# Optimization experiments

Hardware: AMD Instinct MI355X
Metric: run time of the kernel (lower is better)

Reference implementation:

```python
import jax, jax.numpy as jnp
import numpy as np

HIDDEN = 1024
NH = 16
NKV = 8
HD = 128
ROPE_BASE = 1e6
EPS = 1e-6


def _rms_norm(x, w):
    # x: [..., HD], norm in fp32 like the torch module
    xf = x.astype(jnp.float32)
    var = jnp.mean(xf * xf, axis=-1, keepdims=True)
    return w * (xf * jax.lax.rsqrt(var + EPS)).astype(x.dtype)


def _rotate_half(x):
    h = x.shape[-1] // 2
    return jnp.concatenate([-x[..., h:], x[..., :h]], axis=-1)


def _rope_cos_sin(position_ids, dtype):
    inv_freq = 1.0 / (ROPE_BASE ** (jnp.arange(0, HD, 2, dtype=jnp.float32) / HD))
    freqs = position_ids.astype(jnp.float32)[:, None] * inv_freq[None, :]  # [S, HD/2]
    emb = jnp.concatenate([freqs, freqs], axis=-1)  # [S, HD]
    return jnp.cos(emb).astype(dtype), jnp.sin(emb).astype(dtype)


def setup_inputs() -> dict:
    key = jax.random.key(0)
    ks = jax.random.split(key, 7)
    B, S = 2, 2048
    scale = lambda fan_in: 1.0 / np.sqrt(fan_in)
    return {
        "hidden_states": jax.random.normal(ks[0], (B, S, HIDDEN), jnp.float32),
        "position_ids": jnp.arange(S, dtype=jnp.int32),
        "Wq": jax.random.normal(ks[1], (HIDDEN, NH * HD), jnp.float32) * scale(HIDDEN),
        "Wk": jax.random.normal(ks[2], (HIDDEN, NKV * HD), jnp.float32) * scale(HIDDEN),
        "Wv": jax.random.normal(ks[3], (HIDDEN, NKV * HD), jnp.float32) * scale(HIDDEN),
        "Wo": jax.random.normal(ks[4], (NH * HD, HIDDEN), jnp.float32) * scale(NH * HD),
        "q_norm_w": jnp.ones((HD,), jnp.float32),
        "k_norm_w": jnp.ones((HD,), jnp.float32),
    }


def reference(hidden_states, position_ids, Wq, Wk, Wv, Wo, q_norm_w, k_norm_w):
    B, S, _ = hidden_states.shape
    G = NH // NKV  # GQA group size

    q = (hidden_states @ Wq).reshape(B, S, NH, HD)
    k = (hidden_states @ Wk).reshape(B, S, NKV, HD)
    v = (hidden_states @ Wv).reshape(B, S, NKV, HD)

    q = _rms_norm(q, q_norm_w).transpose(0, 2, 1, 3)  # [B, NH, S, HD]
    k = _rms_norm(k, k_norm_w).transpose(0, 2, 1, 3)  # [B, NKV, S, HD]
    v = v.transpose(0, 2, 1, 3)                        # [B, NKV, S, HD]

    cos, sin = _rope_cos_sin(position_ids, q.dtype)    # [S, HD] each
    q = q * cos + _rotate_half(q) * sin
    k = k * cos + _rotate_half(k) * sin

    # GQA: broadcast KV heads across groups instead of repeat_interleave copies
    qg = q.reshape(B, NKV, G, S, HD)
    scores = jnp.einsum('bkgsd,bknd->bkgsn', qg, k) / jnp.sqrt(jnp.float32(HD))
    causal = jnp.tril(jnp.ones((S, S), dtype=bool))
    scores = jnp.where(causal, scores, -jnp.inf)
    attn = jax.nn.softmax(scores, axis=-1)
    out = jnp.einsum('bkgsn,bknd->bkgsd', attn, v)  # [B, NKV, G, S, HD]
    out = out.reshape(B, NH, S, HD).transpose(0, 2, 1, 3).reshape(B, S, NH * HD)
    return out @ Wo
```

## Files before the change

### kernel.cpp

```cpp
#include <hip/hip_runtime.h>
#include <cstdint>
#include <cstddef>

#define HIDDEN 1024
#define NH 16
#define NKV 8
#define HD 128
#define SEQ 2048
#define BATCH 2
#define NTOK (BATCH*SEQ)

typedef __bf16 bf16x8 __attribute__((ext_vector_type(8)));
typedef float f32x4 __attribute__((ext_vector_type(4)));

__device__ __forceinline__ unsigned short f2bf(float f) {
  unsigned int u = __float_as_uint(f);
  u += 0x7FFFu + ((u >> 16) & 1u);
  return (unsigned short)(u >> 16);
}
__device__ __forceinline__ float bf2f(unsigned short h) {
  return __uint_as_float(((unsigned int)h) << 16);
}

#if __has_builtin(__builtin_amdgcn_exp2f)
#define EXP2(x) __builtin_amdgcn_exp2f(x)
#else
#define EXP2(x) exp2f(x)
#endif

__device__ __forceinline__ void glds16(const unsigned short* g, unsigned short* l) {
  __builtin_amdgcn_global_load_lds(
      (const __attribute__((address_space(1))) unsigned int*)g,
      (__attribute__((address_space(3))) unsigned int*)l, 16, 0, 0);
}

#define WAIT_VM8()   __builtin_amdgcn_s_waitcnt(0x0F78)
#define WAIT_VM4()   __builtin_amdgcn_s_waitcnt(0x0F74)
#define WAIT_VM0()   __builtin_amdgcn_s_waitcnt(0x0F70)
#define WAIT_LGKM0() __builtin_amdgcn_s_waitcnt(0xC07F)
#define BARRIER()    __builtin_amdgcn_s_barrier()

__device__ __forceinline__ float dpp_addx1(float x) {
  int v = __builtin_amdgcn_update_dpp(0, __float_as_int(x), 0xB1, 0xF, 0xF, true);
  return x + __int_as_float(v);
}

__global__ __launch_bounds__(256) void tcvt_all_kernel(
    const float* __restrict__ Wq, const float* __restrict__ Wk,
    const float* __restrict__ Wv, const float* __restrict__ Wo,
    const float* __restrict__ hs,
    unsigned short* __restrict__ wqkvt, unsigned short* __restrict__ wot,
    unsigned short* __restrict__ hsb) {
  const int i = blockIdx.x;
  const int tx = threadIdx.x, ty = threadIdx.y;
  if (i >= 6144) {
    const int t = ty*32 + tx;
    const size_t base = (size_t)(i - 6144) * 1024;
#pragma unroll
    for (int j = 0; j < 4; ++j) {
      const size_t idx = base + j*256 + t;
      float4 v = ((const float4*)hs)[idx];
      ushort4 o;
      o.x = f2bf(v.x); o.y = f2bf(v.y); o.z = f2bf(v.z); o.w = f2bf(v.w);
      ((ushort4*)hsb)[idx] = o;
    }
    return;
  }
  __shared__ float tl[32][33];
  const float* src; unsigned short* dst; int R, C, r0, c0;
  if (i < 2048)      { int l = i;        src = Wq; dst = wqkvt;                      R = 1024; C = 2048; r0 = (l & 31)*32; c0 = (l >> 5)*32; }
  else if (i < 3072) { int l = i - 2048; src = Wk; dst = wqkvt + (size_t)2048*1024;  R = 1024; C = 1024; r0 = (l & 31)*32; c0 = (l >> 5)*32; }
  else if (i < 4096) { int l = i - 3072; src = Wv; dst = wqkvt + (size_t)3072*1024;  R = 1024; C = 1024; r0 = (l & 31)*32; c0 = (l >> 5)*32; }
  else               { int l = i - 4096; src = Wo; dst = wot;                        R = 2048; C = 1024; r0 = (l & 63)*32; c0 = (l >> 6)*32; }
#pragma unroll
  for (int k = 0; k < 4; ++k)
    tl[ty + 8*k][tx] = src[(size_t)(r0 + ty + 8*k)*C + c0 + tx];
  __syncthreads();
#pragma unroll
  for (int k = 0; k < 4; ++k)
    dst[(size_t)(c0 + ty + 8*k)*R + r0 + tx] = f2bf(tl[tx][ty + 8*k]);
}

__global__ __launch_bounds__(256) void gemm_qkv_fused_kernel(
    const unsigned short* __restrict__ A,
    const unsigned short* __restrict__ Bt,
    const float* __restrict__ qw, const float* __restrict__ kw,
    const int* __restrict__ pos_ids,
    unsigned short* __restrict__ q_l,
    unsigned short* __restrict__ k_l,
    unsigned short* __restrict__ vt8) {
  constexpr int BM = 128, BK = 64, K = 1024, NIT = K/BK;
  constexpr int FS = 132;
  __shared__ __align__(16) char smem[70144];
  unsigned short* As0 = (unsigned short*)smem;
  unsigned short* Bs0 = (unsigned short*)(smem + 32768);
  float* ftile = (float*)smem;
  float* rinv  = (float*)(smem + 69632);

  const int t = threadIdx.x, lane = t & 63, w = t >> 6;
  const int l15 = lane & 15, l4 = lane >> 4;
  const int wr = (w >> 1)*64, wc = (w & 1)*64;
  const int m0 = blockIdx.x * BM, n0 = blockIdx.y * 128;
  const unsigned short* Ab = A + (size_t)m0*K;
  const unsigned short* Bb = Bt + (size_t)n0*K;

  const f32x4 vzero = {0.f, 0.f, 0.f, 0.f};
  f32x4 acc[4][4];
#pragma unroll
  for (int i = 0; i < 4; ++i)
#pragma unroll
    for (int j = 0; j < 4; ++j) acc[i][j] = vzero;

#pragma unroll
  for (int i = 0; i < 4; ++i) {
    const int c = (w*4 + i)*64 + lane;
    glds16(Ab + (size_t)(c >> 3)*K + (c & 7)*8, As0 + (size_t)(w*4 + i)*512);
  }
#pragma unroll
  for (int i = 0; i < 4; ++i) {
    const int c = (w*4 + i)*64 + lane;
    glds16(Bb + (size_t)(c >> 3)*K + (c & 7)*8, Bs0 + (size_t)(w*4 + i)*512);
  }

  for (int kb = 0; kb < NIT; ++kb) {
    const int cur = kb & 1;
    WAIT_LGKM0(); BARRIER();
    if (kb + 1 < NIT) {
      const int kn = (kb + 1) * BK;
      const int nb = (cur^1)*8192;
#pragma unroll
      for (int i = 0; i < 4; ++i) {
        const int c = (w*4 + i)*64 + lane;
        glds16(Ab + (size_t)(c >> 3)*K + kn + (c & 7)*8, As0 + nb + (size_t)(w*4 + i)*512);
      }
#pragma unroll
      for (int i = 0; i < 4; ++i) {
        const int c = (w*4 + i)*64 + lane;
        glds16(Bb + (size_t)(c >> 3)*K + kn + (c & 7)*8, Bs0 + nb + (size_t)(w*4 + i)*512);
      }
      WAIT_VM8();
    } else {
      WAIT_VM0();
    }
    BARRIER();

    const unsigned short* Ac = As0 + cur*8192;
    const unsigned short* Bc = Bs0 + cur*8192;
#pragma unroll
    for (int kk = 0; kk < 2; ++kk) {
      const int kc = kk*4 + l4;
      bf16x8 af[4], bfr[4];
#pragma unroll
      for (int i = 0; i < 4; ++i) {
        int m = wr + i*16 + l15;
        af[i] = *(const bf16x8*)(Ac + ((size_t)m*8 + kc)*8);
      }
#pragma unroll
      for (int j = 0; j < 4; ++j) {
        int n = wc + j*16 + l15;
        bfr[j] = *(const bf16x8*)(Bc + ((size_t)n*8 + kc)*8);
      }
#pragma unroll
      for (int i = 0; i < 4; ++i)
#pragma unroll
        for (int j = 0; j < 4; ++j)
          acc[i][j] = __builtin_amdgcn_mfma_f32_16x16x32_bf16(af[i], bfr[j], acc[i][j], 0, 0, 0);
    }
  }

  WAIT_LGKM0(); BARRIER();
#pragma unroll
  for (int i = 0; i < 4; ++i)
#pragma unroll
    for (int j = 0; j < 4; ++j)
#pragma unroll
      for (int r = 0; r < 4; ++r) {
        const int row = wr + i*16 + l4*4 + r;
        const int col = wc + j*16 + l15;
        ftile[row*FS + col] = acc[i][j][r];
      }
  WAIT_LGKM0(); BARRIER();

  const int ny = n0 >> 7;
  const int S0 = m0 & (SEQ-1);
  const int bb = m0 >> 11;

  if (ny < 24) {
    const bool isQ = ny < 16;
    {
      const int row = t >> 1, h2 = t & 1;
      const float* fr = ftile + row*FS + h2*64;
      float ssq = 0.f;
#pragma unroll
      for (int c = 0; c < 16; ++c) {
        float4 v = *(const float4*)(fr + 4*c);
        ssq += v.x*v.x + v.y*v.y + v.z*v.z + v.w*v.w;
      }
      ssq = dpp_addx1(ssq);
      if (h2 == 0) rinv[row] = rsqrtf(ssq*(1.0f/128.0f) + 1e-6f);
    }
    WAIT_LGKM0(); BARRIER();
    const float* wgt = isQ ? qw : kw;
    const int d = t & 127, rh = t >> 7;
    const float wd = wgt[d];
    const float w2 = wgt[d ^ 64];
    const float sgn = (d < 64) ? -1.f : 1.f;
    const float sOut = isQ ? 0.12751744f : 1.f;
    const float invf = exp2f(-(float)(d & 63) * 0.31143075889569023f);
    const int pos0 = pos_ids[S0 + rh*64];
    float cs, sn, dc, dsn;
    __sincosf((float)pos0 * invf, &sn, &cs);
    __sincosf(invf, &dsn, &dc);
    const int head = isQ ? ny : (ny - 16);
    unsigned short* dstb = isQ ? (q_l + ((size_t)(bb*NH + head)*SEQ + S0)*HD)
                               : (k_l + ((size_t)(bb*NKV + head)*SEQ + S0)*HD);
#pragma unroll 4
    for (int k = 0; k < 64; ++k) {
      const int row = rh*64 + k;
      const float r  = rinv[row];
      const float x1 = ftile[row*FS + d];
      const float x2 = ftile[row*FS + (d ^ 64)];
      const float y1 = x1*r*wd, y2 = x2*r*w2;
      const float o  = (y1*cs + sgn*(y2*sn)) * sOut;
      dstb[(size_t)row*HD + d] = f2bf(o);
      const float c2 = cs*dc - sn*dsn;
      sn = sn*dc + cs*dsn; cs = c2;
    }
  } else {
    const int vh = ny - 24;
    unsigned short* vb = vt8 + (size_t)(bb*NKV + vh)*HD*SEQ;
    const int d = t & 127, sbh = t >> 7;
#pragma unroll
    for (int sb = 0; sb < 8; ++sb) {
      const int sl = sbh*8 + sb;
      const int blk = sl >> 3, s = sl & 7;
      const int base_r = blk*64 + ((s>>2)<<5) + (((s>>1)&1)<<3) + ((s&1)<<2);
      union { unsigned short u[8]; uint4 q; } pk;
#pragma unroll
      for (int s8 = 0; s8 < 8; ++s8) {
        const int row = base_r + ((s8>>2)<<4) + (((s8>>1)&1)<<1) + (s8&1);
        pk.u[s8] = f2bf(ftile[row*FS + d]);
      }
      *(uint4*)(vb + ((size_t)((S0 >> 3) + sl)*128 + d)*8) = pk.q;
    }
  }
}

__global__ __launch_bounds__(256) void gemm_out_kernel(
    const unsigned short* __restrict__ A,
    const unsigned short* __restrict__ Bt,
    float* __restrict__ Cout, int M, int N, int K) {
  constexpr int BK = 64;
  __shared__ unsigned short As[2][128*BK];
  __shared__ unsigned short Bs[2][128*BK];
  const int t = threadIdx.x, lane = t & 63, w = t >> 6;
  const int l15 = lane & 15, l4 = lane >> 4;
  const int wr = (w >> 1)*64, wc = (w & 1)*64;
  const int m0 = blockIdx.y * 128, n0 = blockIdx.x * 128;
  const unsigned short* Ab = A + (size_t)m0*K;
  const unsigned short* Bb = Bt + (size_t)n0*K;

  const f32x4 vzero = {0.f, 0.f, 0.f, 0.f};
  f32x4 acc[4][4];
#pragma unroll
  for (int i = 0; i < 4; ++i)
#pragma unroll
    for (int j = 0; j < 4; ++j) acc[i][j] = vzero;

  const int NIT = K / BK;
#pragma unroll
  for (int i = 0; i < 4; ++i) {
    const int c = (w*4 + i)*64 + lane;
    glds16(Ab + (size_t)(c >> 3)*K + (c & 7)*8, &As[0][(size_t)(w*4 + i)*512]);
  }
#pragma unroll
  for (int i = 0; i < 4; ++i) {
    const int c = (w*4 + i)*64 + lane;
    glds16(Bb + (size_t)(c >> 3)*K + (c & 7)*8, &Bs[0][(size_t)(w*4 + i)*512]);
  }

  for (int kb = 0; kb < NIT; ++kb) {
    const int cur = kb & 1;
    WAIT_LGKM0(); BARRIER();
    if (kb + 1 < NIT) {
      const int kn = (kb + 1) * BK;
#pragma unroll
      for (int i = 0; i < 4; ++i) {
        const int c = (w*4 + i)*64 + lane;
        glds16(Ab + (size_t)(c >> 3)*K + kn + (c & 7)*8, &As[cur^1][(size_t)(w*4 + i)*512]);
      }
#pragma unroll
      for (int i = 0; i < 4; ++i) {
        const int c = (w*4 + i)*64 + lane;
        glds16(Bb + (size_t)(c >> 3)*K + kn + (c & 7)*8, &Bs[cur^1][(size_t)(w*4 + i)*512]);
      }
      WAIT_VM8();
    } else {
      WAIT_VM0();
    }
    BARRIER();

#pragma unroll
    for (int kk = 0; kk < 2; ++kk) {
      const int kc = kk*4 + l4;
      bf16x8 af[4], bfr[4];
#pragma unroll
      for (int i = 0; i < 4; ++i) {
        int m = wr + i*16 + l15;
        af[i] = *(const bf16x8*)(&As[cur][((size_t)m*8 + kc)*8]);
      }
#pragma unroll
      for (int j = 0; j < 4; ++j) {
        int n = wc + j*16 + l15;
        bfr[j] = *(const bf16x8*)(&Bs[cur][((size_t)n*8 + kc)*8]);
      }
#pragma unroll
      for (int i = 0; i < 4; ++i)
#pragma unroll
        for (int j = 0; j < 4; ++j)
          acc[i][j] = __builtin_amdgcn_mfma_f32_16x16x32_bf16(af[i], bfr[j], acc[i][j], 0, 0, 0);
    }
  }
#pragma unroll
  for (int i = 0; i < 4; ++i)
#pragma unroll
    for (int j = 0; j < 4; ++j)
#pragma unroll
      for (int r = 0; r < 4; ++r) {
        int row = m0 + wr + i*16 + l4*4 + r;
        int col = n0 + wc + j*16 + l15;
        Cout[(size_t)row*N + col] = acc[i][j][r];
      }
}

__global__ __launch_bounds__(256, 2) void attn_kernel(
    const unsigned short* __restrict__ q_l,
    const unsigned short* __restrict__ k_l,
    const unsigned short* __restrict__ vt8,
    unsigned short* __restrict__ o_part,
    float* __restrict__ l_part) {
  __shared__ __align__(16) char smem[65536];
  unsigned short* Ks0  = (unsigned short*)smem;
  unsigned short* Vts0 = (unsigned short*)(smem + 32768);

  const int t = threadIdx.x;
  const int lane = t & 63;
  const int w = t >> 6;
  const int l15 = lane & 15, l4 = lane >> 4;
  const int hb = blockIdx.x;
  const int h = hb & 15, b = hb >> 4;
  const int y = blockIdx.y;
  const int qt = 15 - (y >> 1);
  const int half = y & 1;
  const int kvh = h >> 1;
  const int q0 = qt * 128;
  const int kt0 = half ? (qt + 1) : 0;
  const int kt1 = half ? (2*qt + 2) : (qt + 1);

  const unsigned short* Kg = k_l + ((size_t)(b*NKV + kvh)*SEQ)*HD;
  const unsigned short* Vg = vt8 + (size_t)(b*NKV + kvh)*HD*SEQ;
  const unsigned short* Qbase = q_l + ((size_t)(b*NH + h)*SEQ)*HD;

  const f32x4 vzero = {0.f,0.f,0.f,0.f};

  bf16x8 qf[2][4];
#pragma unroll
  for (int i = 0; i < 2; ++i) {
    const int row = q0 + w*32 + i*16 + l15;
    const unsigned short* Qp = Qbase + (size_t)row*HD;
#pragma unroll
    for (int kk = 0; kk < 4; ++kk)
      qf[i][kk] = *(const bf16x8*)(Qp + kk*32 + l4*8);
  }

  f32x4 oacc[2][8];
#pragma unroll
  for (int i = 0; i < 2; ++i)
#pragma unroll
    for (int jd = 0; jd < 8; ++jd) oacc[i][jd] = vzero;
  float lrun[2] = {0.f, 0.f};

  {
    const int k00 = kt0 * 64;
#pragma unroll
    for (int i = 0; i < 4; ++i) {
      const int kc = w*4 + i;
      const int m = lane ^ (kc & 7);
      glds16(Kg + (size_t)(k00 + m)*HD + kc*8, Ks0 + (size_t)kc*64*8);
    }
#pragma unroll
    for (int i = 0; i < 4; ++i) {
      const int id = w*4 + i;
      const int skc = id >> 1, hh = id & 1;
      const int d = (hh*64 + lane) ^ skc;
      glds16(Vg + ((size_t)((k00 >> 3) + skc)*128 + d)*8, Vts0 + (size_t)(skc*128 + hh*64)*8);
    }
  }

#pragma unroll 1
  for (int kt = kt0; kt < kt1; ++kt) {
    const int cur = (kt - kt0) & 1;
    const int k0 = kt * 64;
    WAIT_LGKM0(); BARRIER();
    if (kt + 1 < kt1) {
      const int kn = k0 + 64;
      unsigned short* Ksn  = Ks0  + (cur^1)*8192;
      unsigned short* Vtsn = Vts0 + (cur^1)*8192;
#pragma unroll
      for (int i = 0; i < 4; ++i) {
        const int kc = w*4 + i;
        const int m = lane ^ (kc & 7);
        glds16(Kg + (size_t)(kn + m)*HD + kc*8, Ksn + (size_t)kc*64*8);
      }
#pragma unroll
      for (int i = 0; i < 4; ++i) {
        const int id = w*4 + i;
        const int skc = id >> 1, hh = id & 1;
        const int d = (hh*64 + lane) ^ skc;
        glds16(Vg + ((size_t)((kn >> 3) + skc)*128 + d)*8, Vtsn + (size_t)(skc*128 + hh*64)*8);
      }
      WAIT_VM8();
    } else {
      WAIT_VM0();
    }
    BARRIER();

    const unsigned short* KsC  = Ks0  + cur*8192;
    const unsigned short* VtsC = Vts0 + cur*8192;

    f32x4 sacc[4][2];
#pragma unroll
    for (int j = 0; j < 4; ++j)
#pragma unroll
      for (int i = 0; i < 2; ++i) sacc[j][i] = vzero;
    __builtin_amdgcn_s_setprio(1);
#pragma unroll
    for (int kk = 0; kk < 4; ++kk) {
      const int kc = kk*4 + l4;
      bf16x8 kb[4];
#pragma unroll
      for (int j = 0; j < 4; ++j) {
        int n = j*16 + l15;
        kb[j] = *(const bf16x8*)(KsC + ((size_t)kc*64 + (n ^ (kc & 7)))*8);
      }
#pragma unroll
      for (int j = 0; j < 4; ++j)
#pragma unroll
        for (int i = 0; i < 2; ++i)
          sacc[j][i] = __builtin_amdgcn_mfma_f32_16x16x32_bf16(kb[j], qf[i][kk], sacc[j][i], 0,0,0);
    }
    __builtin_amdgcn_s_setprio(0);

    const bool diag = (kt >= 2*qt);
#pragma unroll
    for (int j = 0; j < 4; ++j)
#pragma unroll
      for (int i = 0; i < 2; ++i)
#pragma unroll
        for (int r = 0; r < 4; ++r) {
          float sv = sacc[j][i][r];
          if (diag) {
            const int kvg = k0 + j*16 + l4*4 + r;
            const int qg  = q0 + w*32 + i*16 + l15;
            sv = (kvg > qg) ? -INFINITY : sv;
          }
          float pv = EXP2(sv);
          sacc[j][i][r] = pv;
          lrun[i] += pv;
        }

#pragma unroll
    for (int kk = 0; kk < 2; ++kk) {
      union { unsigned int u[4]; bf16x8 v; } pb[2];
#pragma unroll
      for (int i = 0; i < 2; ++i) {
        const f32x4 t0 = sacc[kk*2][i], t1 = sacc[kk*2+1][i];
        pb[i].u[0] = (__float_as_uint(t0[0]) >> 16) | (__float_as_uint(t0[1]) & 0xFFFF0000u);
        pb[i].u[1] = (__float_as_uint(t0[2]) >> 16) | (__float_as_uint(t0[3]) & 0xFFFF0000u);
        pb[i].u[2] = (__float_as_uint(t1[0]) >> 16) | (__float_as_uint(t1[1]) & 0xFFFF0000u);
        pb[i].u[3] = (__float_as_uint(t1[2]) >> 16) | (__float_as_uint(t1[3]) & 0xFFFF0000u);
      }
      const int s = kk*4 + l4;
      __builtin_amdgcn_s_setprio(1);
#pragma unroll
      for (int td = 0; td < 8; ++td) {
        const int dd = td*16 + l15;
        bf16x8 va = *(const bf16x8*)(VtsC + ((size_t)s*128 + (dd ^ s))*8);
#pragma unroll
        for (int i = 0; i < 2; ++i)
          oacc[i][td] = __builtin_amdgcn_mfma_f32_16x16x32_bf16(va, pb[i].v, oacc[i][td], 0,0,0);
      }
      __builtin_amdgcn_s_setprio(0);
    }
  }

  unsigned short* ob = o_part + ((size_t)half*BATCH*NH*SEQ + (size_t)(b*NH + h)*SEQ)*HD;
  float* lb = l_part + (size_t)half*BATCH*NH*SEQ + (size_t)(b*NH + h)*SEQ;
#pragma unroll
  for (int i = 0; i < 2; ++i) {
    float lsum = lrun[i];
    lsum += __shfl_xor(lsum, 16, 64);
    lsum += __shfl_xor(lsum, 32, 64);
    const float inv = (lsum > 0.f) ? 1.0f / lsum : 0.f;
    const int row = q0 + w*32 + i*16 + l15;
    if (l4 == 0) lb[row] = lsum;
#pragma unroll
    for (int td = 0; td < 8; ++td) {
      union { unsigned int u[2]; uint2 q; } pk;
      const float v0 = oacc[i][td][0]*inv, v1 = oacc[i][td][1]*inv;
      const float v2 = oacc[i][td][2]*inv, v3 = oacc[i][td][3]*inv;
      pk.u[0] = (unsigned int)f2bf(v0) | ((unsigned int)f2bf(v1) << 16);
      pk.u[1] = (unsigned int)f2bf(v2) | ((unsigned int)f2bf(v3) << 16);
      *(uint2*)(ob + (size_t)row*HD + td*16 + l4*4) = pk.q;
    }
  }
}

__global__ __launch_bounds__(256) void combine_kernel(
    const unsigned short* __restrict__ o_part,
    const float* __restrict__ l_part,
    unsigned short* __restrict__ attn_o) {
  const int tid = blockIdx.x * 256 + threadIdx.x;
  const int d8 = tid & 15;
  const int row = tid >> 4;
  const int s = row & (SEQ-1);
  const int bh = row >> 11;
  const int h = bh & 15, b = bh >> 4;
  const float la = l_part[row];
  const float lbv = l_part[BATCH*NH*SEQ + row];
  const float inv = 1.f / (la + lbv);
  const float wa = la * inv, wb = lbv * inv;
  const unsigned short* pa = o_part + (size_t)row*HD + d8*8;
  const unsigned short* pb = pa + (size_t)BATCH*NH*SEQ*HD;
  uint4 ua = *(const uint4*)pa;
  uint4 ub = *(const uint4*)pb;
  const unsigned short* ea = (const unsigned short*)&ua;
  const unsigned short* eb = (const unsigned short*)&ub;
  union { unsigned short u[8]; uint4 q; } o;
#pragma unroll
  for (int k = 0; k < 8; ++k)
    o.u[k] = f2bf(bf2f(ea[k])*wa + bf2f(eb[k])*wb);
  *(uint4*)(attn_o + ((size_t)(b*SEQ + s)*(NH*HD)) + h*HD + d8*8) = o.q;
}

extern "C" void kernel_launch(void* const* d_in, const int* in_sizes, int n_in,
                              void* d_out, int out_size, void* d_ws, size_t ws_size,
                              hipStream_t stream) {
  const float* hs = (const float*)d_in[0];
  const int* pos  = (const int*)d_in[1];
  const float* Wq = (const float*)d_in[2];
  const float* Wk = (const float*)d_in[3];
  const float* Wv = (const float*)d_in[4];
  const float* Wo = (const float*)d_in[5];
  const float* qw = (const float*)d_in[6];
  const float* kw = (const float*)d_in[7];
  float* out = (float*)d_out;
  char* ws = (char*)d_ws;

  unsigned short* attn_o = (unsigned short*)(ws + 0);
  unsigned short* wot    = (unsigned short*)(ws + ((size_t)16 << 20));
  unsigned short* q_l    = (unsigned short*)(ws + ((size_t)20 << 20));
  unsigned short* k_l    = (unsigned short*)(ws + ((size_t)36 << 20));
  unsigned short* vt8    = (unsigned short*)(ws + ((size_t)44 << 20));
  unsigned short* o_part = (unsigned short*)(ws + ((size_t)52 << 20));
  unsigned short* hsb    = (unsigned short*)(ws + ((size_t)52 << 20));
  unsigned short* wqkvt  = (unsigned short*)(ws + ((size_t)60 << 20));
  float*          l_part = (float*)(ws + ((size_t)84 << 20));

  tcvt_all_kernel<<<dim3(7168), dim3(32, 8), 0, stream>>>(Wq, Wk, Wv, Wo, hs, wqkvt, wot, hsb);
  gemm_qkv_fused_kernel<<<dim3(32, 32), dim3(256), 0, stream>>>(hsb, wqkvt, qw, kw, pos, q_l, k_l, vt8);
  attn_kernel<<<dim3(32, 32), dim3(256), 0, stream>>>(q_l, k_l, vt8, o_part, l_part);
  combine_kernel<<<dim3(4096), dim3(256), 0, stream>>>(o_part, l_part, attn_o);
  gemm_out_kernel<<<dim3(8, 32), dim3(256), 0, stream>>>(attn_o, wot, out, 4096, 1024, 2048);
}
```

Before: 255.5 us.

## Compute softmax row sums via MFMA with ones and interleave exp with PV

Replaces the per-element VALU accumulation of softmax row sums with an extra MFMA per chunk that multiplies the bf16 probabilities by a ones vector. This yields the row sum directly and removes the cross-lane shuffle reduction at the end. It also splits the exp computation into two halves so the second half's exponentials can overlap with the first half's PV MFMAs. The row sum now comes from bf16-truncated probabilities, consistent with what feeds PV, at the cost of two extra MFMAs per 32-key chunk.

```diff
diff --git a/kernel.cpp b/kernel.cpp
--- a/kernel.cpp
+++ b/kernel.cpp
@@ -362,6 +362,9 @@
   const unsigned short* Qbase = q_l + ((size_t)(b*NH + h)*SEQ)*HD;
 
   const f32x4 vzero = {0.f,0.f,0.f,0.f};
+  union { unsigned int u[4]; bf16x8 v; } vones;
+#pragma unroll
+  for (int i = 0; i < 4; ++i) vones.u[i] = 0x3F803F80u;
 
   bf16x8 qf[2][4];
 #pragma unroll
@@ -378,7 +381,9 @@
   for (int i = 0; i < 2; ++i)
 #pragma unroll
     for (int jd = 0; jd < 8; ++jd) oacc[i][jd] = vzero;
-  float lrun[2] = {0.f, 0.f};
+  f32x4 oextra[2];
+#pragma unroll
+  for (int i = 0; i < 2; ++i) oextra[i] = vzero;
 
   {
     const int k00 = kt0 * 64;
@@ -453,7 +458,7 @@
 
     const bool diag = (kt >= 2*qt);
 #pragma unroll
-    for (int j = 0; j < 4; ++j)
+    for (int j = 0; j < 2; ++j)
 #pragma unroll
       for (int i = 0; i < 2; ++i)
 #pragma unroll
@@ -464,23 +469,20 @@
             const int qg  = q0 + w*32 + i*16 + l15;
             sv = (kvg > qg) ? -INFINITY : sv;
           }
-          float pv = EXP2(sv);
-          sacc[j][i][r] = pv;
-          lrun[i] += pv;
+          sacc[j][i][r] = EXP2(sv);
         }
 
-#pragma unroll
-    for (int kk = 0; kk < 2; ++kk) {
+    {
       union { unsigned int u[4]; bf16x8 v; } pb[2];
 #pragma unroll
       for (int i = 0; i < 2; ++i) {
-        const f32x4 t0 = sacc[kk*2][i], t1 = sacc[kk*2+1][i];
+        const f32x4 t0 = sacc[0][i], t1 = sacc[1][i];
         pb[i].u[0] = (__float_as_uint(t0[0]) >> 16) | (__float_as_uint(t0[1]) & 0xFFFF0000u);
         pb[i].u[1] = (__float_as_uint(t0[2]) >> 16) | (__float_as_uint(t0[3]) & 0xFFFF0000u);
         pb[i].u[2] = (__float_as_uint(t1[0]) >> 16) | (__float_as_uint(t1[1]) & 0xFFFF0000u);
         pb[i].u[3] = (__float_as_uint(t1[2]) >> 16) | (__float_as_uint(t1[3]) & 0xFFFF0000u);
       }
-      const int s = kk*4 + l4;
+      const int s = l4;
       __builtin_amdgcn_s_setprio(1);
 #pragma unroll
       for (int td = 0; td < 8; ++td) {
@@ -490,6 +492,50 @@
         for (int i = 0; i < 2; ++i)
           oacc[i][td] = __builtin_amdgcn_mfma_f32_16x16x32_bf16(va, pb[i].v, oacc[i][td], 0,0,0);
       }
+#pragma unroll
+      for (int i = 0; i < 2; ++i)
+        oextra[i] = __builtin_amdgcn_mfma_f32_16x16x32_bf16(vones.v, pb[i].v, oextra[i], 0,0,0);
+      __builtin_amdgcn_s_setprio(0);
+
+#pragma unroll
+      for (int j = 2; j < 4; ++j)
+#pragma unroll
+        for (int i = 0; i < 2; ++i)
+#pragma unroll
+          for (int r = 0; r < 4; ++r) {
+            float sv = sacc[j][i][r];
+            if (diag) {
+              const int kvg = k0 + j*16 + l4*4 + r;
+              const int qg  = q0 + w*32 + i*16 + l15;
+              sv = (kvg > qg) ? -INFINITY : sv;
+            }
+            sacc[j][i][r] = EXP2(sv);
+          }
+    }
+
+    {
+      union { unsigned int u[4]; bf16x8 v; } pb[2];
+#pragma unroll
+      for (int i = 0; i < 2; ++i) {
+        const f32x4 t0 = sacc[2][i], t1 = sacc[3][i];
+        pb[i].u[0] = (__float_as_uint(t0[0]) >> 16) | (__float_as_uint(t0[1]) & 0xFFFF0000u);
+        pb[i].u[1] = (__float_as_uint(t0[2]) >> 16) | (__float_as_uint(t0[3]) & 0xFFFF0000u);
+        pb[i].u[2] = (__float_as_uint(t1[0]) >> 16) | (__float_as_uint(t1[1]) & 0xFFFF0000u);
+        pb[i].u[3] = (__float_as_uint(t1[2]) >> 16) | (__float_as_uint(t1[3]) & 0xFFFF0000u);
+      }
+      const int s = 4 + l4;
+      __builtin_amdgcn_s_setprio(1);
+#pragma unroll
+      for (int td = 0; td < 8; ++td) {
+        const int dd = td*16 + l15;
+        bf16x8 va = *(const bf16x8*)(VtsC + ((size_t)s*128 + (dd ^ s))*8);
+#pragma unroll
+        for (int i = 0; i < 2; ++i)
+          oacc[i][td] = __builtin_amdgcn_mfma_f32_16x16x32_bf16(va, pb[i].v, oacc[i][td], 0,0,0);
+      }
+#pragma unroll
+      for (int i = 0; i < 2; ++i)
+        oextra[i] = __builtin_amdgcn_mfma_f32_16x16x32_bf16(vones.v, pb[i].v, oextra[i], 0,0,0);
       __builtin_amdgcn_s_setprio(0);
     }
   }
@@ -498,9 +544,7 @@
   float* lb = l_part + (size_t)half*BATCH*NH*SEQ + (size_t)(b*NH + h)*SEQ;
 #pragma unroll
   for (int i = 0; i < 2; ++i) {
-    float lsum = lrun[i];
-    lsum += __shfl_xor(lsum, 16, 64);
-    lsum += __shfl_xor(lsum, 32, 64);
+    const float lsum = oextra[i][0];
     const float inv = (lsum > 0.f) ? 1.0f / lsum : 0.f;
     const int row = q0 + w*32 + i*16 + l15;
     if (l4 == 0) lb[row] = lsum;
```

Measured after the change: 256.5 us. No clear change (+0.4%).
